# Kernel tuning notes

Measured on AMD Instinct MI355X. Metric: run time of the kernel, lower is better.

The kernel has to match this reference:

```python
import jax, jax.numpy as jnp
import numpy as np

EMBED = 256; NH = 8; NP = 32; STRIDE = 4; FFN = 1024
NUM_IMG = 4; H = 160; W = 160; NOBJ = 2048
HD = EMBED // NH
LN_EPS = 1e-5


def setup_inputs():
    key = jax.random.key(0)
    ks = jax.random.split(key, 16)
    inp = {}
    inp["query"] = jax.random.normal(ks[0], (NOBJ, NH, 1, HD), jnp.float32)
    inp["obj_emb"] = jax.random.normal(ks[1], (NOBJ, EMBED), jnp.float32)
    inp["key_feat"] = jax.random.normal(ks[2], (NUM_IMG, EMBED, H, W), jnp.float32)
    inp["value"] = jax.random.normal(ks[3], (NUM_IMG, EMBED, H, W), jnp.float32)
    ys, xs = jnp.meshgrid(jnp.arange(H, dtype=jnp.float32), jnp.arange(W, dtype=jnp.float32), indexing="ij")
    x2d = jnp.stack([(xs + 0.5) * STRIDE, (ys + 0.5) * STRIDE], axis=0)  # (2,H,W) pixel coords
    inp["img_dense_x2d"] = jnp.broadcast_to(x2d[None], (NUM_IMG, 2, H, W)).astype(jnp.float32)
    inp["img_dense_x2d_mask"] = (jax.random.uniform(ks[4], (NUM_IMG, 1, H, W)) > 0.1).astype(jnp.float32)
    inp["obj_xy_point"] = jax.random.uniform(ks[5], (NOBJ, 2)) * jnp.array([W * STRIDE, H * STRIDE], jnp.float32)
    inp["strides"] = 2.0 ** jax.random.randint(ks[6], (NOBJ,), 2, 5).astype(jnp.float32)  # {4,8,16}
    inp["obj_img_ind"] = jax.random.randint(ks[7], (NOBJ,), 0, NUM_IMG, dtype=jnp.int32)
    s = 1.0 / np.sqrt(EMBED)
    inp["w_off"] = jax.random.uniform(ks[8], (EMBED, NH * NP * 2), minval=-s, maxval=s) * 2.5
    inp["b_off"] = jnp.zeros((NH * NP * 2,), jnp.float32)
    inp["w_out"] = jax.random.uniform(ks[9], (EMBED, EMBED), minval=-s, maxval=s)
    inp["b_out"] = jnp.zeros((EMBED,), jnp.float32)
    inp["ln1_g"] = jnp.ones((EMBED,), jnp.float32)
    inp["ln1_b"] = jnp.zeros((EMBED,), jnp.float32)
    inp["w1"] = jax.random.uniform(ks[10], (EMBED, FFN), minval=-s, maxval=s)
    inp["b1"] = jnp.zeros((FFN,), jnp.float32)
    sf = 1.0 / np.sqrt(FFN)
    inp["w2"] = jax.random.uniform(ks[11], (FFN, EMBED), minval=-sf, maxval=sf)
    inp["b2"] = jnp.zeros((EMBED,), jnp.float32)
    inp["ln2_g"] = jnp.ones((EMBED,), jnp.float32)
    inp["ln2_b"] = jnp.zeros((EMBED,), jnp.float32)
    return inp


def _unnorm(g, size):
    # align_corners=False: pixel index = ((g+1)*size - 1) / 2
    return ((g + 1.0) * size - 1.0) * 0.5


def _bilinear(gather, gx, gy, w_size, h_size, zeros_pad):
    """Bilinear sample. gather(y,x) -> (..., C). border or zeros padding."""
    ix = _unnorm(gx, w_size)
    iy = _unnorm(gy, h_size)
    x0f = jnp.floor(ix); y0f = jnp.floor(iy)
    wx1 = ix - x0f; wy1 = iy - y0f
    x0 = x0f.astype(jnp.int32); y0 = y0f.astype(jnp.int32)
    out = None
    for dx, dy, wgt in ((0, 0, (1 - wx1) * (1 - wy1)), (1, 0, wx1 * (1 - wy1)),
                        (0, 1, (1 - wx1) * wy1), (1, 1, wx1 * wy1)):
        xi = x0 + dx; yi = y0 + dy
        xc = jnp.clip(xi, 0, w_size - 1); yc = jnp.clip(yi, 0, h_size - 1)
        if zeros_pad:
            valid = (xi >= 0) & (xi < w_size) & (yi >= 0) & (yi < h_size)
            wgt = wgt * valid.astype(wgt.dtype)
        term = gather(yc, xc) * wgt[..., None]
        out = term if out is None else out + term
    return out


def _ln(x, g, b):
    m = x.mean(-1, keepdims=True)
    v = jnp.mean(jnp.square(x - m), axis=-1, keepdims=True)
    return (x - m) * jax.lax.rsqrt(v + LN_EPS) * g + b


def _forward(query, obj_emb, key_feat, value, img_dense_x2d, img_dense_x2d_mask,
             obj_xy_point, strides, obj_img_ind,
             w_off, b_off, w_out, b_out, ln1_g, ln1_b, w1, b1, w2, b2, ln2_g, ln2_b):
    N = query.shape[0]
    offsets = (obj_emb @ w_off + b_off).reshape(N, NH, NP, 2)
    loc = obj_xy_point[:, None, None] + offsets * strides[:, None, None, None]  # (N,NH,NP,2)
    gx = loc[..., 0] * (2.0 / (W * STRIDE)) - 1.0
    gy = loc[..., 1] * (2.0 / (H * STRIDE)) - 1.0
    # z grid coordinate lands exactly on slice obj_img_ind (zero depth fraction),
    # so 3D trilinear grid_sample reduces to 2D bilinear on the selected image.
    img = obj_img_ind[:, None, None]          # (N,1,1)
    head = jnp.arange(NH)[None, :, None]      # (1,NH,1)
    key_r = key_feat.reshape(NUM_IMG, NH, HD, H, W)
    val_r = value.reshape(NUM_IMG, NH, HD, H, W)
    k_s = _bilinear(lambda y, x: key_r[img, head, :, y, x], gx, gy, W, H, False)   # (N,NH,NP,HD)
    v_s = _bilinear(lambda y, x: val_r[img, head, :, y, x], gx, gy, W, H, False)   # (N,NH,NP,HD)
    x2d_s = _bilinear(lambda y, x: img_dense_x2d[img, :, y, x], gx, gy, W, H, False)       # (N,NH,NP,2)
    mask_s = _bilinear(lambda y, x: img_dense_x2d_mask[img, :, y, x], gx, gy, W, H, True)  # (N,NH,NP,1)
    q = query[:, :, 0]  # (N,NH,HD)
    a = jnp.einsum('nhd,nhpd->nhp', q, k_s) / np.sqrt(HD)
    a_sm = jax.nn.softmax(a, axis=-1) * mask_s[..., 0]
    out = jnp.einsum('nhpd,nhp->nhd', v_s, a_sm).reshape(N, EMBED)
    out = out @ w_out + b_out + obj_emb
    out = _ln(out, ln1_g, ln1_b)
    out = out + (jax.nn.relu(out @ w1 + b1) @ w2 + b2)
    out = _ln(out, ln2_g, ln2_b)
    v_samples = jnp.swapaxes(v_s, -1, -2)      # (N,NH,HD,NP)
    a_samples = a[:, :, None, :]               # (N,NH,1,NP)
    mask_samples = jnp.swapaxes(mask_s, -1, -2)  # (N,NH,1,NP)
    x2d_samples = jnp.swapaxes(x2d_s, -1, -2)    # (N,NH,2,NP)
    return (out, v_samples, a_samples, mask_samples, x2d_samples)


def reference(query, obj_emb, key_feat, value, img_dense_x2d, img_dense_x2d_mask,
              obj_xy_point, strides, obj_img_ind,
              w_off, b_off, w_out, b_out, ln1_g, ln1_b, w1, b1, w2, b2, ln2_g, ln2_b):
    return _forward(query, obj_emb, key_feat, value, img_dense_x2d, img_dense_x2d_mask,
                    obj_xy_point, strides, obj_img_ind,
                    w_off, b_off, w_out, b_out, ln1_g, ln1_b, w1, b1, w2, b2, ln2_g, ln2_b)
```

## Files before the change

### kernel.cpp

```cpp
#include <hip/hip_runtime.h>
#include <hip/hip_fp16.h>
#include <math.h>

#define NOBJ  2048
#define EMBED 256
#define NHD   8
#define NPT   32
#define HD    32
#define NUMIMG 4
#define HH    160
#define WW    160
#define FFN   1024
#define PLANE (HH*WW)
#define LN_EPS 1e-5f

typedef _Float16 f16x8 __attribute__((ext_vector_type(8)));
typedef float f32x4 __attribute__((ext_vector_type(4)));

__global__ __launch_bounds__(256) void k_offsets(
    const float* __restrict__ obj_emb, const float* __restrict__ w_off,
    const float* __restrict__ b_off, const float* __restrict__ obj_xy,
    const float* __restrict__ strides,
    float* __restrict__ cx, float* __restrict__ cy) {
  const int G = 8;
  __shared__ float s_emb[G][EMBED];
  const int t = threadIdx.x;
  const int n0 = blockIdx.x * G;
  #pragma unroll
  for (int g = 0; g < G; ++g) s_emb[g][t] = obj_emb[(n0 + g) * EMBED + t];
  __syncthreads();

  float ax[G], ay[G];
  #pragma unroll
  for (int g = 0; g < G; ++g) { ax[g] = 0.f; ay[g] = 0.f; }

  const float2* wp = (const float2*)w_off;
  for (int e = 0; e < EMBED; ++e) {
    float2 w = wp[e * 256 + t];
    #pragma unroll
    for (int g = 0; g < G; ++g) {
      float a = s_emb[g][e];
      ax[g] = fmaf(a, w.x, ax[g]);
      ay[g] = fmaf(a, w.y, ay[g]);
    }
  }
  const float bx = b_off[2 * t], by = b_off[2 * t + 1];
  #pragma unroll
  for (int g = 0; g < G; ++g) {
    const int n = n0 + g;
    const float st = strides[n];
    const float lx = obj_xy[2 * n]     + (ax[g] + bx) * st;
    const float ly = obj_xy[2 * n + 1] + (ay[g] + by) * st;
    const float gx = lx * (2.0f / (WW * 4)) - 1.0f;
    const float gy = ly * (2.0f / (HH * 4)) - 1.0f;
    const float ix = ((gx + 1.0f) * WW - 1.0f) * 0.5f;
    const float iy = ((gy + 1.0f) * HH - 1.0f) * 0.5f;
    cx[n * 256 + t] = ix;
    cy[n * 256 + t] = iy;
  }
}

__global__ __launch_bounds__(512) void k_relayout(
    const float* __restrict__ key_feat, const float* __restrict__ value,
    __half* __restrict__ kvh) {
  __shared__ __half s[320][144];
  const int t = threadIdx.x;
  const int Y   = blockIdx.x;
  const int hp  = blockIdx.y;
  const int img = blockIdx.z;
  const int pl  = t >> 2;
  const int q   = t & 3;

  const int sub  = pl & 31;
  const int grp  = pl >> 5;
  const int head = hp * 2 + (grp >> 1);
  const int ch   = head * 32 + sub;
  const float* src = (grp & 1) ? value : key_feat;
  const float* sp  = src + ((size_t)img * 256 + ch) * PLANE
                   + (size_t)Y * 320 + q * 80;
  const int pxq = q * 80;

  #pragma unroll
  for (int i0 = 0; i0 < 20; i0 += 10) {
    float4 r[10];
    #pragma unroll
    for (int i = 0; i < 10; ++i) r[i] = *(const float4*)(sp + (i0 + i) * 4);
    #pragma unroll
    for (int i = 0; i < 10; ++i) {
      const int px = pxq + (i0 + i) * 4;
      s[px + 0][pl] = __float2half(r[i].x);
      s[px + 1][pl] = __float2half(r[i].y);
      s[px + 2][pl] = __float2half(r[i].z);
      s[px + 3][pl] = __float2half(r[i].w);
    }
  }
  __syncthreads();

  const size_t rec = (size_t)img * PLANE + (size_t)Y * 320;
  #pragma unroll
  for (int it = 0; it < 10; ++it) {
    const int flat = it * 512 + t;
    const int px = flat >> 4, j = flat & 15;
    const int4 v = *(const int4*)&s[px][j * 8];
    *(int4*)(kvh + (rec + px) * 512 + hp * 128 + j * 8) = v;
  }
}

__device__ __forceinline__ void acc8(int4 r, float w, float* acc) {
  const __half2* hp = (const __half2*)&r;
  #pragma unroll
  for (int i = 0; i < 4; ++i) {
    const float2 f = __half22float2(hp[i]);
    acc[2 * i]     = fmaf(w, f.x, acc[2 * i]);
    acc[2 * i + 1] = fmaf(w, f.y, acc[2 * i + 1]);
  }
}

__global__ __launch_bounds__(256) void k_sample_hwc(
    const float* __restrict__ query, const __half* __restrict__ kvh,
    const float* __restrict__ x2d, const float* __restrict__ x2d_mask,
    const int* __restrict__ obj_img,
    const float* __restrict__ cx, const float* __restrict__ cy,
    float* __restrict__ o_vs, float* __restrict__ o_as,
    float* __restrict__ o_ms, float* __restrict__ o_x2,
    _Float16* __restrict__ attn_h) {
  __shared__ float s_q[256];
  __shared__ float s_v[NHD * NPT * 33];
  __shared__ float s_asm[256];

  const int n = blockIdx.x;
  const int t = threadIdx.x;
  const int h = t >> 5, p = t & 31;

  s_q[t] = query[n * 256 + t];
  const int img = obj_img[n];
  const float ix = cx[n * 256 + t];
  const float iy = cy[n * 256 + t];

  const float x0f = floorf(ix), y0f = floorf(iy);
  const float wx1 = ix - x0f, wy1 = iy - y0f;
  const int x0 = (int)x0f, y0 = (int)y0f;
  const int x1 = x0 + 1, y1 = y0 + 1;
  const int x0c = min(max(x0, 0), WW - 1), x1c = min(max(x1, 0), WW - 1);
  const int y0c = min(max(y0, 0), HH - 1), y1c = min(max(y1, 0), HH - 1);
  const float w00 = (1.f - wx1) * (1.f - wy1);
  const float w10 = wx1 * (1.f - wy1);
  const float w01 = (1.f - wx1) * wy1;
  const float w11 = wx1 * wy1;
  const int o00 = y0c * WW + x0c, o10 = y0c * WW + x1c;
  const int o01 = y1c * WW + x0c, o11 = y1c * WW + x1c;

  const size_t pb = (size_t)img * PLANE;
  const int4* base = (const int4*)kvh;
  const long b0 = ((long)(pb + o00)) * 64 + h * 8;
  const long b1 = ((long)(pb + o10)) * 64 + h * 8;
  const long b2 = ((long)(pb + o01)) * 64 + h * 8;
  const long b3 = ((long)(pb + o11)) * 64 + h * 8;
  __syncthreads();

  float a_acc = 0.f;
  float* svrow = &s_v[(h * NPT + p) * 33];
  float* vout = o_vs + (size_t)(n * NHD + h) * (HD * NPT) + p;
  #pragma unroll
  for (int ch = 0; ch < 4; ++ch) {
    const int4 k0 = base[b0 + ch],     k1 = base[b1 + ch];
    const int4 k2 = base[b2 + ch],     k3 = base[b3 + ch];
    const int4 v0 = base[b0 + 4 + ch], v1 = base[b1 + 4 + ch];
    const int4 v2 = base[b2 + 4 + ch], v3 = base[b3 + 4 + ch];
    float kc[8] = {0, 0, 0, 0, 0, 0, 0, 0};
    float vc[8] = {0, 0, 0, 0, 0, 0, 0, 0};
    acc8(k0, w00, kc); acc8(k1, w10, kc); acc8(k2, w01, kc); acc8(k3, w11, kc);
    acc8(v0, w00, vc); acc8(v1, w10, vc); acc8(v2, w01, vc); acc8(v3, w11, vc);
    #pragma unroll
    for (int j = 0; j < 8; ++j) {
      const int c = ch * 8 + j;
      a_acc = fmaf(s_q[h * HD + c], kc[j], a_acc);
      svrow[c] = vc[j];
      vout[c * NPT] = vc[j];
    }
  }

  const float a = a_acc * 0.17677669529663687f;
  o_as[n * 256 + t] = a;

  const float* xb0 = x2d + (size_t)img * 2 * PLANE;
  const float* xb1 = xb0 + PLANE;
  const float x2v0 = w00 * xb0[o00] + w10 * xb0[o10] + w01 * xb0[o01] + w11 * xb0[o11];
  const float x2v1 = w00 * xb1[o00] + w10 * xb1[o10] + w01 * xb1[o01] + w11 * xb1[o11];
  o_x2[(size_t)n * 512 + h * 64 + p]      = x2v0;
  o_x2[(size_t)n * 512 + h * 64 + 32 + p] = x2v1;

  const float* mb = x2d_mask + (size_t)img * PLANE;
  const float m00 = (x0 >= 0 && x0 < WW && y0 >= 0 && y0 < HH) ? w00 : 0.f;
  const float m10 = (x1 >= 0 && x1 < WW && y0 >= 0 && y0 < HH) ? w10 : 0.f;
  const float m01 = (x0 >= 0 && x0 < WW && y1 >= 0 && y1 < HH) ? w01 : 0.f;
  const float m11 = (x1 >= 0 && x1 < WW && y1 >= 0 && y1 < HH) ? w11 : 0.f;
  const float m = m00 * mb[o00] + m10 * mb[o10] + m01 * mb[o01] + m11 * mb[o11];
  o_ms[n * 256 + t] = m;

  float mx = a;
  #pragma unroll
  for (int o = 16; o >= 1; o >>= 1) mx = fmaxf(mx, __shfl_xor(mx, o, 32));
  const float ev = expf(a - mx);
  float s = ev;
  #pragma unroll
  for (int o = 16; o >= 1; o >>= 1) s += __shfl_xor(s, o, 32);
  s_asm[t] = ev / s * m;
  __syncthreads();

  const int d = p;
  float o = 0.f;
  const float* svh = &s_v[h * NPT * 33];
  const float* amh = &s_asm[h * NPT];
  #pragma unroll
  for (int pp = 0; pp < NPT; ++pp) o = fmaf(amh[pp], svh[pp * 33 + d], o);
  attn_h[n * 256 + t] = (_Float16)o;
}

__global__ __launch_bounds__(256) void k_cvtw(
    const float* __restrict__ w, _Float16* __restrict__ wT, int K, int N) {
  __shared__ float s[32][33];
  const int t = threadIdx.x;
  const int k0 = blockIdx.x * 32, n0 = blockIdx.y * 32;
  const int nl = t & 31, kg = t >> 5;
  #pragma unroll
  for (int i = 0; i < 4; ++i) {
    const int k = kg * 4 + i;
    s[k][nl] = w[(size_t)(k0 + k) * N + n0 + nl];
  }
  __syncthreads();
  const int kl = t & 31, ng = t >> 5;
  #pragma unroll
  for (int i = 0; i < 4; ++i) {
    const int n = ng * 4 + i;
    wT[(size_t)(n0 + n) * K + k0 + kl] = (_Float16)s[kl][n];
  }
}


__global__ __launch_bounds__(256) void k_gemm_a(
    const _Float16* __restrict__ Ah, const _Float16* __restrict__ BT,
    float* __restrict__ C) {
  const int t = threadIdx.x;
  const int wv = t >> 6, lane = t & 63;
  const int r16 = lane & 15, quad = lane >> 4;
  const int m_base = blockIdx.x * 64 + wv * 16;
  const int n_base = blockIdx.y * 32;
  const _Float16* ap  = Ah + (size_t)(m_base + r16) * 256 + quad * 8;
  const _Float16* bp0 = BT + (size_t)(n_base + r16) * 256 + quad * 8;
  const _Float16* bp1 = bp0 + 16 * 256;
  f32x4 acc0 = {0.f, 0.f, 0.f, 0.f}, acc1 = {0.f, 0.f, 0.f, 0.f};
  #pragma unroll 4
  for (int kc = 0; kc < 256; kc += 32) {
    f16x8 a  = *(const f16x8*)(ap + kc);
    f16x8 b0 = *(const f16x8*)(bp0 + kc);
    f16x8 b1 = *(const f16x8*)(bp1 + kc);
    acc0 = __builtin_amdgcn_mfma_f32_16x16x32_f16(a, b0, acc0, 0, 0, 0);
    acc1 = __builtin_amdgcn_mfma_f32_16x16x32_f16(a, b1, acc1, 0, 0, 0);
  }
  float* cp = C + (size_t)(m_base + quad * 4) * 256 + n_base + r16;
  #pragma unroll
  for (int r = 0; r < 4; ++r) {
    cp[(size_t)r * 256]      = acc0[r];
    cp[(size_t)r * 256 + 16] = acc1[r];
  }
}

__global__ __launch_bounds__(256) void k_gemm_b(
    const _Float16* __restrict__ Ah, const _Float16* __restrict__ BT,
    const float* __restrict__ bias, _Float16* __restrict__ Fh) {
  const int t = threadIdx.x;
  const int wv = t >> 6, lane = t & 63;
  const int r16 = lane & 15, quad = lane >> 4;
  const int m_base = blockIdx.x * 64 + wv * 16;
  const int n_base = blockIdx.y * 32;
  const _Float16* ap  = Ah + (size_t)(m_base + r16) * 256 + quad * 8;
  const _Float16* bp0 = BT + (size_t)(n_base + r16) * 256 + quad * 8;
  const _Float16* bp1 = bp0 + 16 * 256;
  f32x4 acc0 = {0.f, 0.f, 0.f, 0.f}, acc1 = {0.f, 0.f, 0.f, 0.f};
  #pragma unroll 4
  for (int kc = 0; kc < 256; kc += 32) {
    f16x8 a  = *(const f16x8*)(ap + kc);
    f16x8 b0 = *(const f16x8*)(bp0 + kc);
    f16x8 b1 = *(const f16x8*)(bp1 + kc);
    acc0 = __builtin_amdgcn_mfma_f32_16x16x32_f16(a, b0, acc0, 0, 0, 0);
    acc1 = __builtin_amdgcn_mfma_f32_16x16x32_f16(a, b1, acc1, 0, 0, 0);
  }
  const float bb0 = bias[n_base + r16];
  const float bb1 = bias[n_base + 16 + r16];
  _Float16* fp = Fh + (size_t)(m_base + quad * 4) * 1024 + n_base + r16;
  #pragma unroll
  for (int r = 0; r < 4; ++r) {
    fp[(size_t)r * 1024]      = (_Float16)fmaxf(acc0[r] + bb0, 0.f);
    fp[(size_t)r * 1024 + 16] = (_Float16)fmaxf(acc1[r] + bb1, 0.f);
  }
}

__global__ __launch_bounds__(256) void k_gemm_c(
    const _Float16* __restrict__ Ah, const _Float16* __restrict__ BT,
    float* __restrict__ C) {
  const int t = threadIdx.x;
  const int wv = t >> 6, lane = t & 63;
  const int r16 = lane & 15, quad = lane >> 4;
  const int m_base = blockIdx.x * 64 + wv * 16;
  const int n_base = blockIdx.y * 32;
  const _Float16* ap  = Ah + (size_t)(m_base + r16) * 1024 + quad * 8;
  const _Float16* bp0 = BT + (size_t)(n_base + r16) * 1024 + quad * 8;
  const _Float16* bp1 = bp0 + 16 * 1024;
  f32x4 acc0 = {0.f, 0.f, 0.f, 0.f}, acc1 = {0.f, 0.f, 0.f, 0.f};
  #pragma unroll 4
  for (int kc = 0; kc < 1024; kc += 32) {
    f16x8 a  = *(const f16x8*)(ap + kc);
    f16x8 b0 = *(const f16x8*)(bp0 + kc);
    f16x8 b1 = *(const f16x8*)(bp1 + kc);
    acc0 = __builtin_amdgcn_mfma_f32_16x16x32_f16(a, b0, acc0, 0, 0, 0);
    acc1 = __builtin_amdgcn_mfma_f32_16x16x32_f16(a, b1, acc1, 0, 0, 0);
  }
  float* cp = C + (size_t)(m_base + quad * 4) * 256 + n_base + r16;
  #pragma unroll
  for (int r = 0; r < 4; ++r) {
    cp[(size_t)r * 256]      = acc0[r];
    cp[(size_t)r * 256 + 16] = acc1[r];
  }
}

__global__ __launch_bounds__(256) void k_ln1(
    const float* __restrict__ Y1, const float* __restrict__ b_out,
    const float* __restrict__ obj_emb, const float* __restrict__ g,
    const float* __restrict__ b, float* __restrict__ U,
    _Float16* __restrict__ Uh) {
  __shared__ float s_y[8][EMBED + 8];
  const int t = threadIdx.x;
  const int m0 = blockIdx.x * 8;
  const float bo = b_out[t];
  #pragma unroll
  for (int r = 0; r < 8; ++r)
    s_y[r][t] = Y1[(size_t)(m0 + r) * EMBED + t] + bo
                + obj_emb[(size_t)(m0 + r) * EMBED + t];
  __syncthreads();
  const int wv = t >> 6, ln = t & 63;
  #pragma unroll
  for (int k = 0; k < 2; ++k) {
    const int rr = wv * 2 + k;
    const float v0 = s_y[rr][ln], v1 = s_y[rr][ln + 64];
    const float v2 = s_y[rr][ln + 128], v3 = s_y[rr][ln + 192];
    float sum = v0 + v1 + v2 + v3;
    #pragma unroll
    for (int o = 32; o >= 1; o >>= 1) sum += __shfl_xor(sum, o);
    const float mean = sum * (1.0f / EMBED);
    const float d0 = v0 - mean, d1 = v1 - mean, d2 = v2 - mean, d3 = v3 - mean;
    float ss = d0 * d0 + d1 * d1 + d2 * d2 + d3 * d3;
    #pragma unroll
    for (int o = 32; o >= 1; o >>= 1) ss += __shfl_xor(ss, o);
    const float rstd = rsqrtf(ss * (1.0f / EMBED) + LN_EPS);
    const size_t base = (size_t)(m0 + rr) * EMBED;
    const float o0 = d0 * rstd * g[ln]       + b[ln];
    const float o1 = d1 * rstd * g[ln + 64]  + b[ln + 64];
    const float o2 = d2 * rstd * g[ln + 128] + b[ln + 128];
    const float o3 = d3 * rstd * g[ln + 192] + b[ln + 192];
    U[base + ln] = o0;         Uh[base + ln] = (_Float16)o0;
    U[base + ln + 64] = o1;    Uh[base + ln + 64] = (_Float16)o1;
    U[base + ln + 128] = o2;   Uh[base + ln + 128] = (_Float16)o2;
    U[base + ln + 192] = o3;   Uh[base + ln + 192] = (_Float16)o3;
  }
}

__global__ __launch_bounds__(256) void k_ln2(
    const float* __restrict__ Y2, const float* __restrict__ b2,
    const float* __restrict__ U, const float* __restrict__ g,
    const float* __restrict__ b, float* __restrict__ out) {
  __shared__ float s_y[8][EMBED + 8];
  const int t = threadIdx.x;
  const int m0 = blockIdx.x * 8;
  const float bb = b2[t];
  #pragma unroll
  for (int r = 0; r < 8; ++r)
    s_y[r][t] = Y2[(size_t)(m0 + r) * EMBED + t] + bb
                + U[(size_t)(m0 + r) * EMBED + t];
  __syncthreads();
  const int wv = t >> 6, ln = t & 63;
  #pragma unroll
  for (int k = 0; k < 2; ++k) {
    const int rr = wv * 2 + k;
    const float v0 = s_y[rr][ln], v1 = s_y[rr][ln + 64];
    const float v2 = s_y[rr][ln + 128], v3 = s_y[rr][ln + 192];
    float sum = v0 + v1 + v2 + v3;
    #pragma unroll
    for (int o = 32; o >= 1; o >>= 1) sum += __shfl_xor(sum, o);
    const float mean = sum * (1.0f / EMBED);
    const float d0 = v0 - mean, d1 = v1 - mean, d2 = v2 - mean, d3 = v3 - mean;
    float ss = d0 * d0 + d1 * d1 + d2 * d2 + d3 * d3;
    #pragma unroll
    for (int o = 32; o >= 1; o >>= 1) ss += __shfl_xor(ss, o);
    const float rstd = rsqrtf(ss * (1.0f / EMBED) + LN_EPS);
    const size_t base = (size_t)(m0 + rr) * EMBED;
    out[base + ln]       = d0 * rstd * g[ln]       + b[ln];
    out[base + ln + 64]  = d1 * rstd * g[ln + 64]  + b[ln + 64];
    out[base + ln + 128] = d2 * rstd * g[ln + 128] + b[ln + 128];
    out[base + ln + 192] = d3 * rstd * g[ln + 192] + b[ln + 192];
  }
}

extern "C" void kernel_launch(void* const* d_in, const int* in_sizes, int n_in,
                              void* d_out, int out_size, void* d_ws, size_t ws_size,
                              hipStream_t stream) {
  const float* query    = (const float*)d_in[0];
  const float* obj_emb  = (const float*)d_in[1];
  const float* key_feat = (const float*)d_in[2];
  const float* value    = (const float*)d_in[3];
  const float* x2d      = (const float*)d_in[4];
  const float* x2d_mask = (const float*)d_in[5];
  const float* obj_xy   = (const float*)d_in[6];
  const float* strides  = (const float*)d_in[7];
  const int*   obj_img  = (const int*)d_in[8];
  const float* w_off    = (const float*)d_in[9];
  const float* b_off    = (const float*)d_in[10];
  const float* w_out    = (const float*)d_in[11];
  const float* b_out    = (const float*)d_in[12];
  const float* ln1_g    = (const float*)d_in[13];
  const float* ln1_b    = (const float*)d_in[14];
  const float* w1       = (const float*)d_in[15];
  const float* b1       = (const float*)d_in[16];
  const float* w2       = (const float*)d_in[17];
  const float* b2       = (const float*)d_in[18];
  const float* ln2_g    = (const float*)d_in[19];
  const float* ln2_b    = (const float*)d_in[20];

  float* out = (float*)d_out;
  float* o_out = out;
  float* o_vs  = out + 524288;
  float* o_as  = out + 524288 + 16777216;
  float* o_ms  = out + 524288 + 16777216 + 524288;
  float* o_x2  = out + 524288 + 16777216 + 1048576;

  char* wsb = (char*)d_ws;
  __half*    kvh    = (__half*)wsb;
  char* B = wsb + 104857600;
  float*     cx     = (float*)(B);
  float*     Y1     = (float*)(B);
  float*     cy     = (float*)(B + 2097152);
  float*     Y2     = (float*)(B + 2097152);
  float*     U      = (float*)(B + 4194304);
  _Float16*  Fh     = (_Float16*)(B + 6291456);
  _Float16*  attn_h = (_Float16*)(B + 10485760);
  _Float16*  Uh     = (_Float16*)(B + 11534336);
  _Float16*  woT    = (_Float16*)(B + 12582912);
  _Float16*  w1T    = (_Float16*)(B + 12582912 + 131072);
  _Float16*  w2T    = (_Float16*)(B + 12582912 + 131072 + 524288);

  k_offsets<<<NOBJ / 8, 256, 0, stream>>>(obj_emb, w_off, b_off, obj_xy,
                                          strides, cx, cy);
  k_relayout<<<dim3(80, 4, NUMIMG), 512, 0, stream>>>(key_feat, value, kvh);
  k_cvtw<<<dim3(8, 8), 256, 0, stream>>>(w_out, woT, 256, 256);
  k_cvtw<<<dim3(8, 32), 256, 0, stream>>>(w1, w1T, 256, 1024);
  k_cvtw<<<dim3(32, 8), 256, 0, stream>>>(w2, w2T, 1024, 256);
  k_sample_hwc<<<NOBJ, 256, 0, stream>>>(query, kvh, x2d, x2d_mask, obj_img,
                                         cx, cy, o_vs, o_as, o_ms, o_x2,
                                         attn_h);
  k_gemm_a<<<dim3(32, 8), 256, 0, stream>>>(attn_h, woT, Y1);
  k_ln1<<<NOBJ / 8, 256, 0, stream>>>(Y1, b_out, obj_emb, ln1_g, ln1_b, U, Uh);
  k_gemm_b<<<dim3(32, 32), 256, 0, stream>>>(Uh, w1T, b1, Fh);
  k_gemm_c<<<dim3(32, 8), 256, 0, stream>>>(Fh, w2T, Y2);
  k_ln2<<<NOBJ / 8, 256, 0, stream>>>(Y2, b2, U, ln2_g, ln2_b, o_out);
}
```

Measured before the change: 448.9 us.

## Fuse LayerNorms into GEMM epilogues and merge weight conversion launches

The output-projection GEMM and the second FFN GEMM now each compute a full 16-row by 256-column tile per block and apply residual add plus LayerNorm in the epilogue, using cross-wave reductions through shared memory. This removes the separate LN kernels and the fp32 Y1/Y2 round trips through global memory. The three weight transpose-convert launches are merged into one. In exchange, the fused GEMMs launch only 128 blocks, which may leave the GPU underoccupied, especially the K=1024 GEMM.

```diff
diff --git a/kernel.cpp b/kernel.cpp
--- a/kernel.cpp
+++ b/kernel.cpp
@@ -217,11 +217,21 @@
   attn_h[n * 256 + t] = (_Float16)o;
 }
 
-__global__ __launch_bounds__(256) void k_cvtw(
-    const float* __restrict__ w, _Float16* __restrict__ wT, int K, int N) {
+__global__ __launch_bounds__(256) void k_cvtw_all(
+    const float* __restrict__ w_out, const float* __restrict__ w1,
+    const float* __restrict__ w2, _Float16* __restrict__ woT,
+    _Float16* __restrict__ w1T, _Float16* __restrict__ w2T) {
   __shared__ float s[32][33];
-  const int t = threadIdx.x;
-  const int k0 = blockIdx.x * 32, n0 = blockIdx.y * 32;
+  const int id = blockIdx.x;
+  const float* w; _Float16* wT; int K, N, kt, nt;
+  if (id < 64)       { w = w_out; wT = woT; K = 256;  N = 256;
+                       kt = id & 7;  nt = id >> 3; }
+  else if (id < 320) { const int r = id - 64;  w = w1; wT = w1T;
+                       K = 256;  N = 1024; kt = r & 7;  nt = r >> 3; }
+  else               { const int r = id - 320; w = w2; wT = w2T;
+                       K = 1024; N = 256;  kt = r & 31; nt = r >> 5; }
+  const int t = threadIdx.x;
+  const int k0 = kt * 32, n0 = nt * 32;
   const int nl = t & 31, kg = t >> 5;
   #pragma unroll
   for (int i = 0; i < 4; ++i) {
@@ -238,9 +248,105 @@
 }
 
 
-__global__ __launch_bounds__(256) void k_gemm_a(
+__global__ __launch_bounds__(256) void k_gemm_a_ln(
     const _Float16* __restrict__ Ah, const _Float16* __restrict__ BT,
-    float* __restrict__ C) {
+    const float* __restrict__ b_out, const float* __restrict__ obj_emb,
+    const float* __restrict__ g, const float* __restrict__ b,
+    float* __restrict__ U, _Float16* __restrict__ Uh) {
+  __shared__ float s_sum[64];
+  __shared__ float s_sq[64];
+  const int t = threadIdx.x;
+  const int wv = t >> 6, lane = t & 63;
+  const int r16 = lane & 15, quad = lane >> 4;
+  const int m0 = blockIdx.x * 16;
+  const int c0 = wv * 64;
+  const _Float16* ap = Ah + (size_t)(m0 + r16) * 256 + quad * 8;
+  const _Float16* bp = BT + (size_t)(c0 + r16) * 256 + quad * 8;
+  f32x4 acc[4] = {{0.f,0.f,0.f,0.f},{0.f,0.f,0.f,0.f},
+                  {0.f,0.f,0.f,0.f},{0.f,0.f,0.f,0.f}};
+  #pragma unroll 2
+  for (int kc = 0; kc < 256; kc += 32) {
+    f16x8 a = *(const f16x8*)(ap + kc);
+    #pragma unroll
+    for (int nt = 0; nt < 4; ++nt) {
+      f16x8 bf = *(const f16x8*)(bp + nt * 16 * 256 + kc);
+      acc[nt] = __builtin_amdgcn_mfma_f32_16x16x32_f16(a, bf, acc[nt], 0, 0, 0);
+    }
+  }
+  float val[4][4];
+  #pragma unroll
+  for (int nt = 0; nt < 4; ++nt) {
+    const int col = c0 + nt * 16 + r16;
+    const float bo = b_out[col];
+    #pragma unroll
+    for (int r = 0; r < 4; ++r)
+      val[nt][r] = acc[nt][r] + bo
+                 + obj_emb[(size_t)(m0 + quad * 4 + r) * 256 + col];
+  }
+  float rs[4];
+  #pragma unroll
+  for (int r = 0; r < 4; ++r) {
+    rs[r] = val[0][r] + val[1][r] + val[2][r] + val[3][r];
+    #pragma unroll
+    for (int m = 1; m < 16; m <<= 1) rs[r] += __shfl_xor(rs[r], m);
+  }
+  if (r16 < 4) {
+    const float v = (r16 == 0) ? rs[0] : (r16 == 1) ? rs[1]
+                  : (r16 == 2) ? rs[2] : rs[3];
+    s_sum[wv * 16 + quad * 4 + r16] = v;
+  }
+  __syncthreads();
+  float mean[4];
+  #pragma unroll
+  for (int r = 0; r < 4; ++r) {
+    const int rr = quad * 4 + r;
+    mean[r] = (s_sum[rr] + s_sum[16 + rr] + s_sum[32 + rr] + s_sum[48 + rr])
+            * (1.0f / EMBED);
+  }
+  float dv[4][4], sq[4];
+  #pragma unroll
+  for (int r = 0; r < 4; ++r) {
+    float ss = 0.f;
+    #pragma unroll
+    for (int nt = 0; nt < 4; ++nt) {
+      dv[nt][r] = val[nt][r] - mean[r];
+      ss = fmaf(dv[nt][r], dv[nt][r], ss);
+    }
+    #pragma unroll
+    for (int m = 1; m < 16; m <<= 1) ss += __shfl_xor(ss, m);
+    sq[r] = ss;
+  }
+  if (r16 < 4) {
+    const float v = (r16 == 0) ? sq[0] : (r16 == 1) ? sq[1]
+                  : (r16 == 2) ? sq[2] : sq[3];
+    s_sq[wv * 16 + quad * 4 + r16] = v;
+  }
+  __syncthreads();
+  float rstd[4];
+  #pragma unroll
+  for (int r = 0; r < 4; ++r) {
+    const int rr = quad * 4 + r;
+    const float var = (s_sq[rr] + s_sq[16 + rr] + s_sq[32 + rr] + s_sq[48 + rr])
+                    * (1.0f / EMBED);
+    rstd[r] = rsqrtf(var + LN_EPS);
+  }
+  #pragma unroll
+  for (int nt = 0; nt < 4; ++nt) {
+    const int col = c0 + nt * 16 + r16;
+    const float gg = g[col], bb = b[col];
+    #pragma unroll
+    for (int r = 0; r < 4; ++r) {
+      const size_t idx = (size_t)(m0 + quad * 4 + r) * 256 + col;
+      const float u = dv[nt][r] * rstd[r] * gg + bb;
+      U[idx] = u;
+      Uh[idx] = (_Float16)u;
+    }
+  }
+}
+
+__global__ __launch_bounds__(256) void k_gemm_b(
+    const _Float16* __restrict__ Ah, const _Float16* __restrict__ BT,
+    const float* __restrict__ bias, _Float16* __restrict__ Fh) {
   const int t = threadIdx.x;
   const int wv = t >> 6, lane = t & 63;
   const int r16 = lane & 15, quad = lane >> 4;
@@ -258,34 +364,6 @@
     acc0 = __builtin_amdgcn_mfma_f32_16x16x32_f16(a, b0, acc0, 0, 0, 0);
     acc1 = __builtin_amdgcn_mfma_f32_16x16x32_f16(a, b1, acc1, 0, 0, 0);
   }
-  float* cp = C + (size_t)(m_base + quad * 4) * 256 + n_base + r16;
-  #pragma unroll
-  for (int r = 0; r < 4; ++r) {
-    cp[(size_t)r * 256]      = acc0[r];
-    cp[(size_t)r * 256 + 16] = acc1[r];
-  }
-}
-
-__global__ __launch_bounds__(256) void k_gemm_b(
-    const _Float16* __restrict__ Ah, const _Float16* __restrict__ BT,
-    const float* __restrict__ bias, _Float16* __restrict__ Fh) {
-  const int t = threadIdx.x;
-  const int wv = t >> 6, lane = t & 63;
-  const int r16 = lane & 15, quad = lane >> 4;
-  const int m_base = blockIdx.x * 64 + wv * 16;
-  const int n_base = blockIdx.y * 32;
-  const _Float16* ap  = Ah + (size_t)(m_base + r16) * 256 + quad * 8;
-  const _Float16* bp0 = BT + (size_t)(n_base + r16) * 256 + quad * 8;
-  const _Float16* bp1 = bp0 + 16 * 256;
-  f32x4 acc0 = {0.f, 0.f, 0.f, 0.f}, acc1 = {0.f, 0.f, 0.f, 0.f};
-  #pragma unroll 4
-  for (int kc = 0; kc < 256; kc += 32) {
-    f16x8 a  = *(const f16x8*)(ap + kc);
-    f16x8 b0 = *(const f16x8*)(bp0 + kc);
-    f16x8 b1 = *(const f16x8*)(bp1 + kc);
-    acc0 = __builtin_amdgcn_mfma_f32_16x16x32_f16(a, b0, acc0, 0, 0, 0);
-    acc1 = __builtin_amdgcn_mfma_f32_16x16x32_f16(a, b1, acc1, 0, 0, 0);
-  }
   const float bb0 = bias[n_base + r16];
   const float bb1 = bias[n_base + 16 + r16];
   _Float16* fp = Fh + (size_t)(m_base + quad * 4) * 1024 + n_base + r16;
@@ -296,108 +374,95 @@
   }
 }
 
-__global__ __launch_bounds__(256) void k_gemm_c(
+__global__ __launch_bounds__(256) void k_gemm_c_ln(
     const _Float16* __restrict__ Ah, const _Float16* __restrict__ BT,
-    float* __restrict__ C) {
+    const float* __restrict__ b2, const float* __restrict__ Ures,
+    const float* __restrict__ g, const float* __restrict__ b,
+    float* __restrict__ out) {
+  __shared__ float s_sum[64];
+  __shared__ float s_sq[64];
   const int t = threadIdx.x;
   const int wv = t >> 6, lane = t & 63;
   const int r16 = lane & 15, quad = lane >> 4;
-  const int m_base = blockIdx.x * 64 + wv * 16;
-  const int n_base = blockIdx.y * 32;
-  const _Float16* ap  = Ah + (size_t)(m_base + r16) * 1024 + quad * 8;
-  const _Float16* bp0 = BT + (size_t)(n_base + r16) * 1024 + quad * 8;
-  const _Float16* bp1 = bp0 + 16 * 1024;
-  f32x4 acc0 = {0.f, 0.f, 0.f, 0.f}, acc1 = {0.f, 0.f, 0.f, 0.f};
-  #pragma unroll 4
+  const int m0 = blockIdx.x * 16;
+  const int c0 = wv * 64;
+  const _Float16* ap = Ah + (size_t)(m0 + r16) * 1024 + quad * 8;
+  const _Float16* bp = BT + (size_t)(c0 + r16) * 1024 + quad * 8;
+  f32x4 acc[4] = {{0.f,0.f,0.f,0.f},{0.f,0.f,0.f,0.f},
+                  {0.f,0.f,0.f,0.f},{0.f,0.f,0.f,0.f}};
+  #pragma unroll 2
   for (int kc = 0; kc < 1024; kc += 32) {
-    f16x8 a  = *(const f16x8*)(ap + kc);
-    f16x8 b0 = *(const f16x8*)(bp0 + kc);
-    f16x8 b1 = *(const f16x8*)(bp1 + kc);
-    acc0 = __builtin_amdgcn_mfma_f32_16x16x32_f16(a, b0, acc0, 0, 0, 0);
-    acc1 = __builtin_amdgcn_mfma_f32_16x16x32_f16(a, b1, acc1, 0, 0, 0);
-  }
-  float* cp = C + (size_t)(m_base + quad * 4) * 256 + n_base + r16;
-  #pragma unroll
-  for (int r = 0; r < 4; ++r) {
-    cp[(size_t)r * 256]      = acc0[r];
-    cp[(size_t)r * 256 + 16] = acc1[r];
-  }
-}
-
-__global__ __launch_bounds__(256) void k_ln1(
-    const float* __restrict__ Y1, const float* __restrict__ b_out,
-    const float* __restrict__ obj_emb, const float* __restrict__ g,
-    const float* __restrict__ b, float* __restrict__ U,
-    _Float16* __restrict__ Uh) {
-  __shared__ float s_y[8][EMBED + 8];
-  const int t = threadIdx.x;
-  const int m0 = blockIdx.x * 8;
-  const float bo = b_out[t];
-  #pragma unroll
-  for (int r = 0; r < 8; ++r)
-    s_y[r][t] = Y1[(size_t)(m0 + r) * EMBED + t] + bo
-                + obj_emb[(size_t)(m0 + r) * EMBED + t];
-  __syncthreads();
-  const int wv = t >> 6, ln = t & 63;
-  #pragma unroll
-  for (int k = 0; k < 2; ++k) {
-    const int rr = wv * 2 + k;
-    const float v0 = s_y[rr][ln], v1 = s_y[rr][ln + 64];
-    const float v2 = s_y[rr][ln + 128], v3 = s_y[rr][ln + 192];
-    float sum = v0 + v1 + v2 + v3;
-    #pragma unroll
-    for (int o = 32; o >= 1; o >>= 1) sum += __shfl_xor(sum, o);
-    const float mean = sum * (1.0f / EMBED);
-    const float d0 = v0 - mean, d1 = v1 - mean, d2 = v2 - mean, d3 = v3 - mean;
-    float ss = d0 * d0 + d1 * d1 + d2 * d2 + d3 * d3;
-    #pragma unroll
-    for (int o = 32; o >= 1; o >>= 1) ss += __shfl_xor(ss, o);
-    const float rstd = rsqrtf(ss * (1.0f / EMBED) + LN_EPS);
-    const size_t base = (size_t)(m0 + rr) * EMBED;
-    const float o0 = d0 * rstd * g[ln]       + b[ln];
-    const float o1 = d1 * rstd * g[ln + 64]  + b[ln + 64];
-    const float o2 = d2 * rstd * g[ln + 128] + b[ln + 128];
-    const float o3 = d3 * rstd * g[ln + 192] + b[ln + 192];
-    U[base + ln] = o0;         Uh[base + ln] = (_Float16)o0;
-    U[base + ln + 64] = o1;    Uh[base + ln + 64] = (_Float16)o1;
-    U[base + ln + 128] = o2;   Uh[base + ln + 128] = (_Float16)o2;
-    U[base + ln + 192] = o3;   Uh[base + ln + 192] = (_Float16)o3;
-  }
-}
-
-__global__ __launch_bounds__(256) void k_ln2(
-    const float* __restrict__ Y2, const float* __restrict__ b2,
-    const float* __restrict__ U, const float* __restrict__ g,
-    const float* __restrict__ b, float* __restrict__ out) {
-  __shared__ float s_y[8][EMBED + 8];
-  const int t = threadIdx.x;
-  const int m0 = blockIdx.x * 8;
-  const float bb = b2[t];
-  #pragma unroll
-  for (int r = 0; r < 8; ++r)
-    s_y[r][t] = Y2[(size_t)(m0 + r) * EMBED + t] + bb
-                + U[(size_t)(m0 + r) * EMBED + t];
-  __syncthreads();
-  const int wv = t >> 6, ln = t & 63;
-  #pragma unroll
-  for (int k = 0; k < 2; ++k) {
-    const int rr = wv * 2 + k;
-    const float v0 = s_y[rr][ln], v1 = s_y[rr][ln + 64];
-    const float v2 = s_y[rr][ln + 128], v3 = s_y[rr][ln + 192];
-    float sum = v0 + v1 + v2 + v3;
-    #pragma unroll
-    for (int o = 32; o >= 1; o >>= 1) sum += __shfl_xor(sum, o);
-    const float mean = sum * (1.0f / EMBED);
-    const float d0 = v0 - mean, d1 = v1 - mean, d2 = v2 - mean, d3 = v3 - mean;
-    float ss = d0 * d0 + d1 * d1 + d2 * d2 + d3 * d3;
-    #pragma unroll
-    for (int o = 32; o >= 1; o >>= 1) ss += __shfl_xor(ss, o);
-    const float rstd = rsqrtf(ss * (1.0f / EMBED) + LN_EPS);
-    const size_t base = (size_t)(m0 + rr) * EMBED;
-    out[base + ln]       = d0 * rstd * g[ln]       + b[ln];
-    out[base + ln + 64]  = d1 * rstd * g[ln + 64]  + b[ln + 64];
-    out[base + ln + 128] = d2 * rstd * g[ln + 128] + b[ln + 128];
-    out[base + ln + 192] = d3 * rstd * g[ln + 192] + b[ln + 192];
+    f16x8 a = *(const f16x8*)(ap + kc);
+    #pragma unroll
+    for (int nt = 0; nt < 4; ++nt) {
+      f16x8 bf = *(const f16x8*)(bp + nt * 16 * 1024 + kc);
+      acc[nt] = __builtin_amdgcn_mfma_f32_16x16x32_f16(a, bf, acc[nt], 0, 0, 0);
+    }
+  }
+  float val[4][4];
+  #pragma unroll
+  for (int nt = 0; nt < 4; ++nt) {
+    const int col = c0 + nt * 16 + r16;
+    const float bo = b2[col];
+    #pragma unroll
+    for (int r = 0; r < 4; ++r)
+      val[nt][r] = acc[nt][r] + bo
+                 + Ures[(size_t)(m0 + quad * 4 + r) * 256 + col];
+  }
+  float rs[4];
+  #pragma unroll
+  for (int r = 0; r < 4; ++r) {
+    rs[r] = val[0][r] + val[1][r] + val[2][r] + val[3][r];
+    #pragma unroll
+    for (int m = 1; m < 16; m <<= 1) rs[r] += __shfl_xor(rs[r], m);
+  }
+  if (r16 < 4) {
+    const float v = (r16 == 0) ? rs[0] : (r16 == 1) ? rs[1]
+                  : (r16 == 2) ? rs[2] : rs[3];
+    s_sum[wv * 16 + quad * 4 + r16] = v;
+  }
+  __syncthreads();
+  float mean[4];
+  #pragma unroll
+  for (int r = 0; r < 4; ++r) {
+    const int rr = quad * 4 + r;
+    mean[r] = (s_sum[rr] + s_sum[16 + rr] + s_sum[32 + rr] + s_sum[48 + rr])
+            * (1.0f / EMBED);
+  }
+  float dv[4][4], sq[4];
+  #pragma unroll
+  for (int r = 0; r < 4; ++r) {
+    float ss = 0.f;
+    #pragma unroll
+    for (int nt = 0; nt < 4; ++nt) {
+      dv[nt][r] = val[nt][r] - mean[r];
+      ss = fmaf(dv[nt][r], dv[nt][r], ss);
+    }
+    #pragma unroll
+    for (int m = 1; m < 16; m <<= 1) ss += __shfl_xor(ss, m);
+    sq[r] = ss;
+  }
+  if (r16 < 4) {
+    const float v = (r16 == 0) ? sq[0] : (r16 == 1) ? sq[1]
+                  : (r16 == 2) ? sq[2] : sq[3];
+    s_sq[wv * 16 + quad * 4 + r16] = v;
+  }
+  __syncthreads();
+  float rstd[4];
+  #pragma unroll
+  for (int r = 0; r < 4; ++r) {
+    const int rr = quad * 4 + r;
+    const float var = (s_sq[rr] + s_sq[16 + rr] + s_sq[32 + rr] + s_sq[48 + rr])
+                    * (1.0f / EMBED);
+    rstd[r] = rsqrtf(var + LN_EPS);
+  }
+  #pragma unroll
+  for (int nt = 0; nt < 4; ++nt) {
+    const int col = c0 + nt * 16 + r16;
+    const float gg = g[col], bb = b[col];
+    #pragma unroll
+    for (int r = 0; r < 4; ++r)
+      out[(size_t)(m0 + quad * 4 + r) * 256 + col] = dv[nt][r] * rstd[r] * gg + bb;
   }
 }
 
@@ -437,9 +502,7 @@
   __half*    kvh    = (__half*)wsb;
   char* B = wsb + 104857600;
   float*     cx     = (float*)(B);
-  float*     Y1     = (float*)(B);
   float*     cy     = (float*)(B + 2097152);
-  float*     Y2     = (float*)(B + 2097152);
   float*     U      = (float*)(B + 4194304);
   _Float16*  Fh     = (_Float16*)(B + 6291456);
   _Float16*  attn_h = (_Float16*)(B + 10485760);
@@ -451,15 +514,13 @@
   k_offsets<<<NOBJ / 8, 256, 0, stream>>>(obj_emb, w_off, b_off, obj_xy,
                                           strides, cx, cy);
   k_relayout<<<dim3(80, 4, NUMIMG), 512, 0, stream>>>(key_feat, value, kvh);
-  k_cvtw<<<dim3(8, 8), 256, 0, stream>>>(w_out, woT, 256, 256);
-  k_cvtw<<<dim3(8, 32), 256, 0, stream>>>(w1, w1T, 256, 1024);
-  k_cvtw<<<dim3(32, 8), 256, 0, stream>>>(w2, w2T, 1024, 256);
+  k_cvtw_all<<<576, 256, 0, stream>>>(w_out, w1, w2, woT, w1T, w2T);
   k_sample_hwc<<<NOBJ, 256, 0, stream>>>(query, kvh, x2d, x2d_mask, obj_img,
                                          cx, cy, o_vs, o_as, o_ms, o_x2,
                                          attn_h);
-  k_gemm_a<<<dim3(32, 8), 256, 0, stream>>>(attn_h, woT, Y1);
-  k_ln1<<<NOBJ / 8, 256, 0, stream>>>(Y1, b_out, obj_emb, ln1_g, ln1_b, U, Uh);
+  k_gemm_a_ln<<<NOBJ / 16, 256, 0, stream>>>(attn_h, woT, b_out, obj_emb,
+                                             ln1_g, ln1_b, U, Uh);
   k_gemm_b<<<dim3(32, 32), 256, 0, stream>>>(Uh, w1T, b1, Fh);
-  k_gemm_c<<<dim3(32, 8), 256, 0, stream>>>(Fh, w2T, Y2);
-  k_ln2<<<NOBJ / 8, 256, 0, stream>>>(Y2, b2, U, ln2_g, ln2_b, o_out);
-}
+  k_gemm_c_ln<<<NOBJ / 16, 256, 0, stream>>>(Fh, w2T, b2, U, ln2_g, ln2_b,
+                                             o_out);
+}
```

After: 461.6 us. 2.8% more time.
